# Kernel tuning notes

Hardware: AMD Instinct MI355X
Metric: run time of the kernel (lower is better)

## Reference

```python
import jax, jax.numpy as jnp
import numpy as np

N_ITEM = 100000
DIV_TRADEOFF = 0.1


def setup_inputs() -> dict:
    key = jax.random.key(0)
    ks = jax.random.split(key, 9)
    B, K, L, D_LLM, H = 512, 8, 50, 768, 128
    return {
        "user_id": jax.random.randint(ks[0], (B,), 0, 50000),
        "base_model_preds": jax.random.randint(ks[1], (B, K, L), 0, N_ITEM + 1),
        "preference_in": jax.random.normal(ks[2], (B, H), jnp.float32),
        "pos_label": jax.random.normal(ks[3], (B, K), jnp.float32),
        "neg_label": jax.random.normal(ks[4], (B, K), jnp.float32),
        "user_embeddings": jax.random.normal(ks[5], (50000, H), jnp.float32) * 0.01,
        "item_embeddings": jax.random.normal(ks[6], (N_ITEM + 1, D_LLM), jnp.float32) * 0.02,
        "W_proj": jax.random.normal(ks[7], (D_LLM, H), jnp.float32) * (1.0 / np.sqrt(D_LLM)),
        "b_proj": jax.random.normal(ks[8], (H,), jnp.float32) * 0.01,
    }


def reference(user_id, base_model_preds, preference_in, pos_label, neg_label,
              user_embeddings, item_embeddings, W_proj, b_proj):
    B, K, L = base_model_preds.shape
    # masked gather-embed: ids outside (0, n_item] map to a zero row
    valid = (base_model_preds > 0) & (base_model_preds <= N_ITEM)
    safe_ids = jnp.where(valid, base_model_preds, 0)
    focus_llm = item_embeddings[safe_ids] * valid[..., None].astype(item_embeddings.dtype)  # [B,K,L,D_llm]
    # linear projection to hidden (bias applied everywhere, matching nn.Linear on zeroed rows)
    bm = jnp.einsum('bkld,dh->bklh', focus_llm, W_proj) + b_proj  # [B,K,L,H]
    # time-decay weighted sum over sequence positions
    time_w = 1.0 / jnp.log2(jnp.arange(L, dtype=jnp.float32) + 2.0)  # [L]
    basemodel_emb = jnp.einsum('bklh,l->bkh', bm, time_w)  # [B,K,H]
    # preference = DIEN(...) + user_emb  (DIEN output modeled by preference_in)
    preference = preference_in + user_embeddings[user_id]  # [B,H]
    wgts_org = jnp.einsum('bkh,bh->bk', basemodel_emb, preference)
    wgts = jax.nn.softmax(wgts_org, axis=-1)  # [B,K]
    pos_scores = jnp.sum(pos_label * wgts, axis=1)
    neg_scores = jnp.sum(neg_label * wgts, axis=1)
    loss = -jnp.sum(jax.nn.log_sigmoid(pos_scores - neg_scores))
    # diversity regularizer (use_div=True)
    cov_wgt = jax.lax.stop_gradient(wgts[:, None, :] + wgts[:, :, None])  # [B,K,K]
    cov_mask = 1.0 - jnp.eye(K, dtype=wgts.dtype)  # [K,K]
    gram = jnp.einsum('bih,bjh->bij', basemodel_emb, basemodel_emb) ** 2
    loss_div = DIV_TRADEOFF * jnp.mean(cov_mask[None] * gram * cov_wgt)
    return loss + loss_div
```

## Files before the change

kernel.cpp:

```cpp
#include <hip/hip_runtime.h>
#include <math.h>

#define B_SZ 512
#define K_SZ 8
#define L_SZ 50
#define DLLM 768
#define H_SZ 128
#define N_ITEM 100000
#define DIV_TRADEOFF 0.1f
#define M_PAD 100032

typedef float  f32x4 __attribute__((ext_vector_type(4)));
typedef short  bf16x8 __attribute__((ext_vector_type(8)));
typedef unsigned int u32x4 __attribute__((ext_vector_type(4)));
typedef unsigned short u16x8 __attribute__((ext_vector_type(8)));

__device__ __forceinline__ unsigned short f2bf(float f) {
    unsigned u = __float_as_uint(f);
    u += 0x7fffu + ((u >> 16) & 1u);
    return (unsigned short)(u >> 16);
}

__device__ __forceinline__ void gload_lds16(const void* g, void* l) {
    __builtin_amdgcn_global_load_lds(
        (const __attribute__((address_space(1))) unsigned*)g,
        (__attribute__((address_space(3))) unsigned*)l, 16, 0, 0);
}

__global__ __launch_bounds__(256) void k_wt(
    const float* __restrict__ W,
    unsigned short* __restrict__ Wt,
    float* __restrict__ out)
{
    __shared__ float tile[64][65];
    const int kb = blockIdx.x >> 1;
    const int nb = blockIdx.x & 1;
    const int t  = threadIdx.x;
    if (blockIdx.x == 0 && t == 0) out[0] = 0.0f;

    const int r  = t >> 2;
    const int c0 = (t & 3) * 16;
    #pragma unroll
    for (int j = 0; j < 4; ++j) {
        const float4 v = *(const float4*)(W + (size_t)(kb * 64 + r) * H_SZ + nb * 64 + c0 + j * 4);
        tile[r][c0 + j * 4 + 0] = v.x;
        tile[r][c0 + j * 4 + 1] = v.y;
        tile[r][c0 + j * 4 + 2] = v.z;
        tile[r][c0 + j * 4 + 3] = v.w;
    }
    __syncthreads();
    const int n  = t >> 2;
    const int k0 = (t & 3) * 16;
    u16x8 lo, hi;
    #pragma unroll
    for (int j = 0; j < 8; ++j) lo[j] = f2bf(tile[k0 + j][n]);
    #pragma unroll
    for (int j = 0; j < 8; ++j) hi[j] = f2bf(tile[k0 + 8 + j][n]);
    unsigned short* dst = Wt + (size_t)(nb * 64 + n) * DLLM + kb * 64 + k0;
    *(u16x8*)(dst)     = lo;
    *(u16x8*)(dst + 8) = hi;
}

__global__ __launch_bounds__(256) void k_proj(
    const float* __restrict__ item,
    const unsigned short* __restrict__ Wt,
    unsigned short* __restrict__ projb)
{
    __shared__ float          As[2][64 * 64];
    __shared__ unsigned short Bs[2][128 * 64];

    const int t    = threadIdx.x;
    const int brow = blockIdx.x * 64;
    const int w    = t >> 6;
    const int lane = t & 63;
    const int nl   = lane & 15;
    const int g    = lane >> 4;
    const int key  = nl & 7;

    const int a_rsub = (lane >> 4);
    const int a_gl   = lane & 15;
    const int b_nsub = (lane >> 3);
    const int b_gl   = lane & 7;
    const int b_key  = b_nsub & 7;

    const int r = w * 16 + nl;

    auto STAGE = [&](int d, int c) {
        const int kc = c * 64;
        #pragma unroll
        for (int i = 0; i < 4; ++i) {
            const int row_t = w * 16 + i * 4 + a_rsub;
            const int rowS  = (brow + row_t <= N_ITEM) ? (brow + row_t) : N_ITEM;
            const int ka    = (a_gl ^ (row_t & 7)) * 4;
            gload_lds16(item + (size_t)rowS * DLLM + kc + ka,
                        &As[d][w * 1024 + i * 256]);
        }
        #pragma unroll
        for (int i = 0; i < 4; ++i) {
            const int n_t = w * 32 + i * 8 + b_nsub;
            const int kb  = (b_gl ^ b_key) * 8;
            gload_lds16(Wt + (size_t)n_t * DLLM + kc + kb,
                        &Bs[d][w * 2048 + i * 512]);
        }
    };

    f32x4 acc[8];
    #pragma unroll
    for (int i = 0; i < 8; ++i) acc[i] = (f32x4){0.f, 0.f, 0.f, 0.f};

    STAGE(0, 0);

    for (int c = 0; c < 12; ++c) {
        const int cur = c & 1;
        if (c < 11) STAGE(cur ^ 1, c + 1);
        if (c < 11) asm volatile("s_waitcnt vmcnt(8)" ::: "memory");
        else        asm volatile("s_waitcnt vmcnt(0)" ::: "memory");
        __builtin_amdgcn_s_barrier();
        __builtin_amdgcn_sched_barrier(0);

        #pragma unroll
        for (int ks = 0; ks < 2; ++ks) {
            const f32x4 alo = *(const f32x4*)&As[cur][r * 64 + 4 * ((ks * 8 + 2 * g)     ^ key)];
            const f32x4 ahi = *(const f32x4*)&As[cur][r * 64 + 4 * ((ks * 8 + 2 * g + 1) ^ key)];
            unsigned p0, p1, p2, p3;
            asm("v_cvt_pk_bf16_f32 %0, %1, %2" : "=v"(p0) : "v"(alo.x), "v"(alo.y));
            asm("v_cvt_pk_bf16_f32 %0, %1, %2" : "=v"(p1) : "v"(alo.z), "v"(alo.w));
            asm("v_cvt_pk_bf16_f32 %0, %1, %2" : "=v"(p2) : "v"(ahi.x), "v"(ahi.y));
            asm("v_cvt_pk_bf16_f32 %0, %1, %2" : "=v"(p3) : "v"(ahi.z), "v"(ahi.w));
            union { u32x4 u; bf16x8 s; } af;
            af.u[0] = p0; af.u[1] = p1; af.u[2] = p2; af.u[3] = p3;

            #pragma unroll
            for (int nt = 0; nt < 8; ++nt) {
                const bf16x8 b = *(const bf16x8*)&Bs[cur][(nt * 16 + nl) * 64
                                                          + 8 * ((ks * 4 + g) ^ key)];
                acc[nt] = __builtin_amdgcn_mfma_f32_16x16x32_bf16(af.s, b, acc[nt], 0, 0, 0);
            }
        }
        asm volatile("s_waitcnt lgkmcnt(0)" ::: "memory");
        __builtin_amdgcn_s_barrier();
        __builtin_amdgcn_sched_barrier(0);
    }

    const int rbase = brow + w * 16 + 4 * g;
    #pragma unroll
    for (int nt = 0; nt < 8; ++nt) {
        #pragma unroll
        for (int rr = 0; rr < 4; ++rr) {
            projb[(size_t)(rbase + rr) * H_SZ + nt * 16 + nl] = f2bf(acc[nt][rr]);
        }
    }
}

__global__ __launch_bounds__(256) void k_gather2(
    const int* __restrict__ preds,
    const unsigned short* __restrict__ projb,
    const float* __restrict__ bproj,
    float* __restrict__ emb)
{
    const int wv   = threadIdx.x >> 6;
    const int lane = threadIdx.x & 63;
    const int bk   = blockIdx.x * 4 + wv;
    const int h2   = lane * 2;
    const int* __restrict__ p = preds + (size_t)bk * L_SZ;

    constexpr int PF = 8;
    unsigned buf[PF];
    float wgt[PF];
    #pragma unroll
    for (int i = 0; i < PF; ++i) {
        const int id = p[i];
        const bool v = (id > 0) && (id <= N_ITEM);
        wgt[i] = v ? (1.0f / log2f((float)(i + 2))) : 0.0f;
        buf[i] = *(const unsigned*)(projb + (size_t)(v ? id : 0) * H_SZ + h2);
    }
    float a0 = 0.f, a1 = 0.f;
    #pragma unroll
    for (int l = 0; l < L_SZ; ++l) {
        const int s = l % PF;
        const unsigned u = buf[s];
        const float w = wgt[s];
        if (l + PF < L_SZ) {
            const int id = p[l + PF];
            const bool v = (id > 0) && (id <= N_ITEM);
            wgt[s] = v ? (1.0f / log2f((float)(l + PF + 2))) : 0.0f;
            buf[s] = *(const unsigned*)(projb + (size_t)(v ? id : 0) * H_SZ + h2);
        }
        a0 += w * __uint_as_float(u << 16);
        a1 += w * __uint_as_float(u & 0xffff0000u);
    }
    float sumw = 0.f;
    #pragma unroll
    for (int l = 0; l < L_SZ; ++l) sumw += 1.0f / log2f((float)(l + 2));
    float2 o;
    o.x = a0 + bproj[h2]     * sumw;
    o.y = a1 + bproj[h2 + 1] * sumw;
    *(float2*)(emb + (size_t)bk * H_SZ + h2) = o;
}

__global__ __launch_bounds__(256) void k_loss(
    const int* __restrict__ user_id, const float* __restrict__ pref_in,
    const float* __restrict__ pos_label, const float* __restrict__ neg_label,
    const float* __restrict__ user_emb, const float* __restrict__ emb,
    float* __restrict__ out)
{
    const int b = blockIdx.x;
    const int tid = threadIdx.x;
    __shared__ float pref[H_SZ];
    __shared__ float e[K_SZ][H_SZ + 1];
    __shared__ float sdot[K_SZ];
    __shared__ float wg[K_SZ];
    __shared__ float lossb_s;
    if (tid < H_SZ) {
        const int uid = user_id[b];
        pref[tid] = pref_in[(size_t)b * H_SZ + tid] + user_emb[(size_t)uid * H_SZ + tid];
    }
    const float* eb = emb + (size_t)b * K_SZ * H_SZ;
    #pragma unroll
    for (int i = 0; i < 4; ++i) {
        const int idx = tid * 4 + i;
        e[idx >> 7][idx & (H_SZ - 1)] = eb[idx];
    }
    __syncthreads();
    {
        const int k = tid >> 5;
        const int lane = tid & 31;
        float s = e[k][lane] * pref[lane] + e[k][lane + 32] * pref[lane + 32]
                + e[k][lane + 64] * pref[lane + 64] + e[k][lane + 96] * pref[lane + 96];
        #pragma unroll
        for (int m = 16; m >= 1; m >>= 1) s += __shfl_xor(s, m, 64);
        if (lane == 0) sdot[k] = s;
    }
    __syncthreads();
    if (tid == 0) {
        float mx = sdot[0];
        #pragma unroll
        for (int k = 1; k < K_SZ; ++k) mx = fmaxf(mx, sdot[k]);
        float sum = 0.f; float ex[K_SZ];
        #pragma unroll
        for (int k = 0; k < K_SZ; ++k) { ex[k] = expf(sdot[k] - mx); sum += ex[k]; }
        float ps = 0.f, ns = 0.f;
        #pragma unroll
        for (int k = 0; k < K_SZ; ++k) {
            const float w = ex[k] / sum;
            wg[k] = w;
            ps += pos_label[(size_t)b * K_SZ + k] * w;
            ns += neg_label[(size_t)b * K_SZ + k] * w;
        }
        const float x = ps - ns;
        lossb_s = fmaxf(-x, 0.f) + log1pf(expf(-fabsf(x)));
    }
    __syncthreads();
    if (tid < 64) {
        const int i = tid >> 3;
        const int j = tid & 7;
        float g = 0.f;
        for (int h = 0; h < H_SZ; ++h) g += e[i][h] * e[j][h];
        float v = (i != j) ? (g * g * (wg[i] + wg[j])) : 0.f;
        #pragma unroll
        for (int m = 32; m >= 1; m >>= 1) v += __shfl_xor(v, m, 64);
        if (tid == 0) {
            const float mean_div = v / (float)(B_SZ * K_SZ * K_SZ);
            atomicAdd(out, lossb_s + DIV_TRADEOFF * mean_div);
        }
    }
}

__global__ __launch_bounds__(192) void k_gather_fb(
    const int* __restrict__ preds, const float* __restrict__ item,
    float* __restrict__ wf, float* __restrict__ out)
{
    const int bk  = blockIdx.x;
    const int tid = threadIdx.x;
    if (bk == 0 && tid == 0) out[0] = 0.0f;
    const int* __restrict__ p = preds + (size_t)bk * L_SZ;
    const float* __restrict__ ibase = item + (size_t)tid * 4;
    float4 acc = make_float4(0.f, 0.f, 0.f, 0.f);
    constexpr int PF = 8;
    float4 buf[PF]; float wgt[PF];
    #pragma unroll
    for (int i = 0; i < PF; ++i) {
        const int id = p[i];
        const bool v = (id > 0) && (id <= N_ITEM);
        wgt[i] = v ? (1.0f / log2f((float)(i + 2))) : 0.0f;
        buf[i] = *(const float4*)(ibase + (size_t)(v ? id : 0) * DLLM);
    }
    #pragma unroll
    for (int l = 0; l < L_SZ; ++l) {
        const int s = l % PF;
        const float4 v4 = buf[s];
        const float  w  = wgt[s];
        if (l + PF < L_SZ) {
            const int id = p[l + PF];
            const bool v = (id > 0) && (id <= N_ITEM);
            wgt[s] = v ? (1.0f / log2f((float)(l + PF + 2))) : 0.0f;
            buf[s] = *(const float4*)(ibase + (size_t)(v ? id : 0) * DLLM);
        }
        acc.x += w * v4.x; acc.y += w * v4.y; acc.z += w * v4.z; acc.w += w * v4.w;
    }
    *(float4*)(wf + (size_t)bk * DLLM + (size_t)tid * 4) = acc;
}

__global__ __launch_bounds__(256) void k_projloss_fb(
    const float* __restrict__ wf, const float* __restrict__ W,
    const float* __restrict__ bproj, const int* __restrict__ user_id,
    const float* __restrict__ pref_in, const float* __restrict__ pos_label,
    const float* __restrict__ neg_label, const float* __restrict__ user_emb,
    float* __restrict__ out)
{
    const int b   = blockIdx.x;
    const int tid = threadIdx.x;
    const int c   = tid & (H_SZ - 1);
    const int rg  = tid >> 7;
    __shared__ float A[K_SZ][H_SZ];
    __shared__ float e[K_SZ][H_SZ + 1];
    __shared__ float pref[H_SZ];
    __shared__ float sdot[K_SZ];
    __shared__ float wg[K_SZ];
    __shared__ float lossb_s;
    float acc[4] = {0.f, 0.f, 0.f, 0.f};
    const size_t rowbase = (size_t)b * K_SZ;
    for (int kb = 0; kb < DLLM; kb += H_SZ) {
        __syncthreads();
        {
            const int r  = tid >> 5;
            const int kk = (tid & 31) * 4;
            *(float4*)&A[r][kk] = *(const float4*)(wf + (rowbase + r) * DLLM + kb + kk);
        }
        __syncthreads();
        #pragma unroll 4
        for (int k = 0; k < H_SZ; k += 4) {
            const float4 a0 = *(const float4*)&A[rg][k];
            const float4 a1 = *(const float4*)&A[rg + 2][k];
            const float4 a2 = *(const float4*)&A[rg + 4][k];
            const float4 a3 = *(const float4*)&A[rg + 6][k];
            const float* Wp = W + (size_t)(kb + k) * H_SZ + c;
            const float w0 = Wp[0]; const float w1 = Wp[H_SZ];
            const float w2 = Wp[2 * H_SZ]; const float w3 = Wp[3 * H_SZ];
            acc[0] += a0.x * w0 + a0.y * w1 + a0.z * w2 + a0.w * w3;
            acc[1] += a1.x * w0 + a1.y * w1 + a1.z * w2 + a1.w * w3;
            acc[2] += a2.x * w0 + a2.y * w1 + a2.z * w2 + a2.w * w3;
            acc[3] += a3.x * w0 + a3.y * w1 + a3.z * w2 + a3.w * w3;
        }
    }
    float sumw = 0.f;
    #pragma unroll
    for (int l = 0; l < L_SZ; ++l) sumw += 1.0f / log2f((float)(l + 2));
    const float bterm = bproj[c] * sumw;
    #pragma unroll
    for (int ri = 0; ri < 4; ++ri) e[rg + 2 * ri][c] = acc[ri] + bterm;
    if (tid < H_SZ) {
        const int uid = user_id[b];
        pref[tid] = pref_in[(size_t)b * H_SZ + tid] + user_emb[(size_t)uid * H_SZ + tid];
    }
    __syncthreads();
    {
        const int k    = tid >> 5;
        const int lane = tid & 31;
        float s = e[k][lane] * pref[lane] + e[k][lane + 32] * pref[lane + 32]
                + e[k][lane + 64] * pref[lane + 64] + e[k][lane + 96] * pref[lane + 96];
        #pragma unroll
        for (int m = 16; m >= 1; m >>= 1) s += __shfl_xor(s, m, 64);
        if (lane == 0) sdot[k] = s;
    }
    __syncthreads();
    if (tid == 0) {
        float mx = sdot[0];
        #pragma unroll
        for (int k = 1; k < K_SZ; ++k) mx = fmaxf(mx, sdot[k]);
        float sum = 0.f; float ex[K_SZ];
        #pragma unroll
        for (int k = 0; k < K_SZ; ++k) { ex[k] = expf(sdot[k] - mx); sum += ex[k]; }
        float ps = 0.f, ns = 0.f;
        #pragma unroll
        for (int k = 0; k < K_SZ; ++k) {
            const float w = ex[k] / sum;
            wg[k] = w;
            ps += pos_label[(size_t)b * K_SZ + k] * w;
            ns += neg_label[(size_t)b * K_SZ + k] * w;
        }
        const float x = ps - ns;
        lossb_s = fmaxf(-x, 0.f) + log1pf(expf(-fabsf(x)));
    }
    __syncthreads();
    if (tid < 64) {
        const int i = tid >> 3;
        const int j = tid & 7;
        float g = 0.f;
        for (int h = 0; h < H_SZ; ++h) g += e[i][h] * e[j][h];
        float v = (i != j) ? (g * g * (wg[i] + wg[j])) : 0.f;
        #pragma unroll
        for (int m = 32; m >= 1; m >>= 1) v += __shfl_xor(v, m, 64);
        if (tid == 0) {
            const float mean_div = v / (float)(B_SZ * K_SZ * K_SZ);
            atomicAdd(out, lossb_s + DIV_TRADEOFF * mean_div);
        }
    }
}

extern "C" void kernel_launch(void* const* d_in, const int* in_sizes, int n_in,
                              void* d_out, int out_size, void* d_ws, size_t ws_size,
                              hipStream_t stream) {
    const int*   user_id   = (const int*)  d_in[0];
    const int*   preds     = (const int*)  d_in[1];
    const float* pref_in   = (const float*)d_in[2];
    const float* pos_label = (const float*)d_in[3];
    const float* neg_label = (const float*)d_in[4];
    const float* user_emb  = (const float*)d_in[5];
    const float* item_emb  = (const float*)d_in[6];
    const float* W_proj    = (const float*)d_in[7];
    const float* b_proj    = (const float*)d_in[8];

    float* out = (float*)d_out;

    const size_t projb_bytes = (size_t)M_PAD * H_SZ * sizeof(unsigned short);
    const size_t wt_off      = projb_bytes;
    const size_t wt_bytes    = (size_t)H_SZ * DLLM * sizeof(unsigned short);
    const size_t emb_off     = wt_off + wt_bytes;
    const size_t emb_bytes   = (size_t)B_SZ * K_SZ * H_SZ * sizeof(float);
    const size_t need        = emb_off + emb_bytes;

    if (ws_size >= need) {
        unsigned short* projb = (unsigned short*)d_ws;
        unsigned short* Wt    = (unsigned short*)((char*)d_ws + wt_off);
        float*          emb   = (float*)((char*)d_ws + emb_off);

        k_wt<<<24, 256, 0, stream>>>(W_proj, Wt, out);
        k_proj<<<M_PAD / 64, 256, 0, stream>>>(item_emb, Wt, projb);
        k_gather2<<<B_SZ * K_SZ / 4, 256, 0, stream>>>(preds, projb, b_proj, emb);
        k_loss<<<B_SZ, 256, 0, stream>>>(user_id, pref_in, pos_label, neg_label,
                                         user_emb, emb, out);
    } else {
        float* wf = (float*)d_ws;
        k_gather_fb<<<B_SZ * K_SZ, 192, 0, stream>>>(preds, item_emb, wf, out);
        k_projloss_fb<<<B_SZ, 256, 0, stream>>>(wf, W_proj, b_proj, user_id, pref_in,
                                                pos_label, neg_label, user_emb, out);
    }
}
```

Before: 107.8 us.

## Preload bf16 A tile once per block in k_proj and fuse gather with loss

k_proj now loads the full 32-row slice of item embeddings up front, converts it to bf16 once and keeps all of K in LDS. This removes the per-k-step fp32 A staging and repeated conversions, and the block now uses 32 rows with four waves splitting the N dimension. The gather and loss kernels are fused into one 512-thread block per batch row, which drops the intermediate emb buffer and one launch. The trade-offs are a larger LDS footprint per block, less overlap of A loads with compute, and a higher occupancy target of two blocks per CU.

```diff
diff --git a/kernel.cpp b/kernel.cpp
--- a/kernel.cpp
+++ b/kernel.cpp
@@ -61,40 +61,28 @@
     *(u16x8*)(dst + 8) = hi;
 }
 
-__global__ __launch_bounds__(256) void k_proj(
+__global__ __launch_bounds__(256, 2) void k_proj(
     const float* __restrict__ item,
     const unsigned short* __restrict__ Wt,
     unsigned short* __restrict__ projb)
 {
-    __shared__ float          As[2][64 * 64];
+    __shared__ unsigned short As[32 * DLLM];
     __shared__ unsigned short Bs[2][128 * 64];
 
     const int t    = threadIdx.x;
-    const int brow = blockIdx.x * 64;
+    const int brow = blockIdx.x * 32;
     const int w    = t >> 6;
     const int lane = t & 63;
     const int nl   = lane & 15;
     const int g    = lane >> 4;
     const int key  = nl & 7;
 
-    const int a_rsub = (lane >> 4);
-    const int a_gl   = lane & 15;
     const int b_nsub = (lane >> 3);
     const int b_gl   = lane & 7;
     const int b_key  = b_nsub & 7;
 
-    const int r = w * 16 + nl;
-
-    auto STAGE = [&](int d, int c) {
+    auto STAGE_B = [&](int d, int c) {
         const int kc = c * 64;
-        #pragma unroll
-        for (int i = 0; i < 4; ++i) {
-            const int row_t = w * 16 + i * 4 + a_rsub;
-            const int rowS  = (brow + row_t <= N_ITEM) ? (brow + row_t) : N_ITEM;
-            const int ka    = (a_gl ^ (row_t & 7)) * 4;
-            gload_lds16(item + (size_t)rowS * DLLM + kc + ka,
-                        &As[d][w * 1024 + i * 256]);
-        }
         #pragma unroll
         for (int i = 0; i < 4; ++i) {
             const int n_t = w * 32 + i * 8 + b_nsub;
@@ -104,37 +92,55 @@
         }
     };
 
-    f32x4 acc[8];
-    #pragma unroll
-    for (int i = 0; i < 8; ++i) acc[i] = (f32x4){0.f, 0.f, 0.f, 0.f};
-
-    STAGE(0, 0);
+    STAGE_B(0, 0);
+
+    {
+        f32x4 L[24];
+        #pragma unroll
+        for (int j = 0; j < 24; ++j) {
+            const int row_g = brow + w * 8 + j / 3;
+            const int rowS  = (row_g <= N_ITEM) ? row_g : N_ITEM;
+            L[j] = *(const f32x4*)(item + (size_t)rowS * DLLM + (j % 3) * 256 + lane * 4);
+        }
+        #pragma unroll
+        for (int j = 0; j < 24; ++j) {
+            unsigned p0, p1;
+            asm("v_cvt_pk_bf16_f32 %0, %1, %2" : "=v"(p0) : "v"(L[j].x), "v"(L[j].y));
+            asm("v_cvt_pk_bf16_f32 %0, %1, %2" : "=v"(p1) : "v"(L[j].z), "v"(L[j].w));
+            const int row_l = w * 8 + j / 3;
+            const int rk    = (j / 3) & 7;
+            const int pos   = (j % 3) * 32 + ((lane >> 1) ^ rk);
+            uint2 d; d.x = p0; d.y = p1;
+            *(uint2*)((char*)As + row_l * (DLLM * 2) + pos * 16 + (lane & 1) * 8) = d;
+        }
+    }
+    __syncthreads();
+
+    const int arow = (w & 1) * 16 + nl;
+    const int nth  = (w >> 1) * 4;
+
+    f32x4 acc[4];
+    #pragma unroll
+    for (int i = 0; i < 4; ++i) acc[i] = (f32x4){0.f, 0.f, 0.f, 0.f};
 
     for (int c = 0; c < 12; ++c) {
         const int cur = c & 1;
-        if (c < 11) STAGE(cur ^ 1, c + 1);
-        if (c < 11) asm volatile("s_waitcnt vmcnt(8)" ::: "memory");
+        if (c < 11) STAGE_B(cur ^ 1, c + 1);
+        if (c < 11) asm volatile("s_waitcnt vmcnt(4)" ::: "memory");
         else        asm volatile("s_waitcnt vmcnt(0)" ::: "memory");
         __builtin_amdgcn_s_barrier();
         __builtin_amdgcn_sched_barrier(0);
 
         #pragma unroll
         for (int ks = 0; ks < 2; ++ks) {
-            const f32x4 alo = *(const f32x4*)&As[cur][r * 64 + 4 * ((ks * 8 + 2 * g)     ^ key)];
-            const f32x4 ahi = *(const f32x4*)&As[cur][r * 64 + 4 * ((ks * 8 + 2 * g + 1) ^ key)];
-            unsigned p0, p1, p2, p3;
-            asm("v_cvt_pk_bf16_f32 %0, %1, %2" : "=v"(p0) : "v"(alo.x), "v"(alo.y));
-            asm("v_cvt_pk_bf16_f32 %0, %1, %2" : "=v"(p1) : "v"(alo.z), "v"(alo.w));
-            asm("v_cvt_pk_bf16_f32 %0, %1, %2" : "=v"(p2) : "v"(ahi.x), "v"(ahi.y));
-            asm("v_cvt_pk_bf16_f32 %0, %1, %2" : "=v"(p3) : "v"(ahi.z), "v"(ahi.w));
-            union { u32x4 u; bf16x8 s; } af;
-            af.u[0] = p0; af.u[1] = p1; af.u[2] = p2; af.u[3] = p3;
-
+            const int q = (ks * 4 + g) ^ key;
+            const bf16x8 af = *(const bf16x8*)((char*)As
+                                + arow * (DLLM * 2) + (c * 8 + q) * 16);
             #pragma unroll
-            for (int nt = 0; nt < 8; ++nt) {
-                const bf16x8 b = *(const bf16x8*)&Bs[cur][(nt * 16 + nl) * 64
-                                                          + 8 * ((ks * 4 + g) ^ key)];
-                acc[nt] = __builtin_amdgcn_mfma_f32_16x16x32_bf16(af.s, b, acc[nt], 0, 0, 0);
+            for (int nt = 0; nt < 4; ++nt) {
+                const bf16x8 b = *(const bf16x8*)&Bs[cur][((nth + nt) * 16 + nl) * 64
+                                                          + 8 * q];
+                acc[nt] = __builtin_amdgcn_mfma_f32_16x16x32_bf16(af, b, acc[nt], 0, 0, 0);
             }
         }
         asm volatile("s_waitcnt lgkmcnt(0)" ::: "memory");
@@ -142,96 +148,87 @@
         __builtin_amdgcn_sched_barrier(0);
     }
 
-    const int rbase = brow + w * 16 + 4 * g;
-    #pragma unroll
-    for (int nt = 0; nt < 8; ++nt) {
+    const int rbase = brow + (w & 1) * 16 + 4 * g;
+    #pragma unroll
+    for (int nt = 0; nt < 4; ++nt) {
         #pragma unroll
         for (int rr = 0; rr < 4; ++rr) {
-            projb[(size_t)(rbase + rr) * H_SZ + nt * 16 + nl] = f2bf(acc[nt][rr]);
-        }
-    }
-}
-
-__global__ __launch_bounds__(256) void k_gather2(
+            projb[(size_t)(rbase + rr) * H_SZ + (nth + nt) * 16 + nl] = f2bf(acc[nt][rr]);
+        }
+    }
+}
+
+__global__ __launch_bounds__(512) void k_gloss(
     const int* __restrict__ preds,
     const unsigned short* __restrict__ projb,
     const float* __restrict__ bproj,
-    float* __restrict__ emb)
-{
-    const int wv   = threadIdx.x >> 6;
-    const int lane = threadIdx.x & 63;
-    const int bk   = blockIdx.x * 4 + wv;
-    const int h2   = lane * 2;
-    const int* __restrict__ p = preds + (size_t)bk * L_SZ;
-
-    constexpr int PF = 8;
-    unsigned buf[PF];
-    float wgt[PF];
-    #pragma unroll
-    for (int i = 0; i < PF; ++i) {
-        const int id = p[i];
-        const bool v = (id > 0) && (id <= N_ITEM);
-        wgt[i] = v ? (1.0f / log2f((float)(i + 2))) : 0.0f;
-        buf[i] = *(const unsigned*)(projb + (size_t)(v ? id : 0) * H_SZ + h2);
-    }
-    float a0 = 0.f, a1 = 0.f;
-    #pragma unroll
-    for (int l = 0; l < L_SZ; ++l) {
-        const int s = l % PF;
-        const unsigned u = buf[s];
-        const float w = wgt[s];
-        if (l + PF < L_SZ) {
-            const int id = p[l + PF];
-            const bool v = (id > 0) && (id <= N_ITEM);
-            wgt[s] = v ? (1.0f / log2f((float)(l + PF + 2))) : 0.0f;
-            buf[s] = *(const unsigned*)(projb + (size_t)(v ? id : 0) * H_SZ + h2);
-        }
-        a0 += w * __uint_as_float(u << 16);
-        a1 += w * __uint_as_float(u & 0xffff0000u);
-    }
-    float sumw = 0.f;
-    #pragma unroll
-    for (int l = 0; l < L_SZ; ++l) sumw += 1.0f / log2f((float)(l + 2));
-    float2 o;
-    o.x = a0 + bproj[h2]     * sumw;
-    o.y = a1 + bproj[h2 + 1] * sumw;
-    *(float2*)(emb + (size_t)bk * H_SZ + h2) = o;
-}
-
-__global__ __launch_bounds__(256) void k_loss(
     const int* __restrict__ user_id, const float* __restrict__ pref_in,
     const float* __restrict__ pos_label, const float* __restrict__ neg_label,
-    const float* __restrict__ user_emb, const float* __restrict__ emb,
+    const float* __restrict__ user_emb,
     float* __restrict__ out)
 {
-    const int b = blockIdx.x;
-    const int tid = threadIdx.x;
+    const int b    = blockIdx.x;
+    const int tid  = threadIdx.x;
+    const int wv   = tid >> 6;
+    const int lane = tid & 63;
+    const int h2   = lane * 2;
+
+    __shared__ float e[K_SZ][H_SZ + 1];
     __shared__ float pref[H_SZ];
-    __shared__ float e[K_SZ][H_SZ + 1];
     __shared__ float sdot[K_SZ];
     __shared__ float wg[K_SZ];
     __shared__ float lossb_s;
+
+    {
+        const int* __restrict__ p = preds + ((size_t)b * K_SZ + wv) * L_SZ;
+        constexpr int PF = 8;
+        unsigned buf[PF];
+        float wgt[PF];
+        #pragma unroll
+        for (int i = 0; i < PF; ++i) {
+            const int id = p[i];
+            const bool v = (id > 0) && (id <= N_ITEM);
+            wgt[i] = v ? (1.0f / log2f((float)(i + 2))) : 0.0f;
+            buf[i] = *(const unsigned*)(projb + (size_t)(v ? id : 0) * H_SZ + h2);
+        }
+        float a0 = 0.f, a1 = 0.f;
+        #pragma unroll
+        for (int l = 0; l < L_SZ; ++l) {
+            const int s = l % PF;
+            const unsigned u = buf[s];
+            const float w = wgt[s];
+            if (l + PF < L_SZ) {
+                const int id = p[l + PF];
+                const bool v = (id > 0) && (id <= N_ITEM);
+                wgt[s] = v ? (1.0f / log2f((float)(l + PF + 2))) : 0.0f;
+                buf[s] = *(const unsigned*)(projb + (size_t)(v ? id : 0) * H_SZ + h2);
+            }
+            a0 += w * __uint_as_float(u << 16);
+            a1 += w * __uint_as_float(u & 0xffff0000u);
+        }
+        float sumw = 0.f;
+        #pragma unroll
+        for (int l = 0; l < L_SZ; ++l) sumw += 1.0f / log2f((float)(l + 2));
+        e[wv][h2]     = a0 + bproj[h2]     * sumw;
+        e[wv][h2 + 1] = a1 + bproj[h2 + 1] * sumw;
+    }
     if (tid < H_SZ) {
         const int uid = user_id[b];
         pref[tid] = pref_in[(size_t)b * H_SZ + tid] + user_emb[(size_t)uid * H_SZ + tid];
     }
-    const float* eb = emb + (size_t)b * K_SZ * H_SZ;
-    #pragma unroll
-    for (int i = 0; i < 4; ++i) {
-        const int idx = tid * 4 + i;
-        e[idx >> 7][idx & (H_SZ - 1)] = eb[idx];
-    }
-    __syncthreads();
-    {
+    __syncthreads();
+
+    if (tid < 256) {
         const int k = tid >> 5;
-        const int lane = tid & 31;
-        float s = e[k][lane] * pref[lane] + e[k][lane + 32] * pref[lane + 32]
-                + e[k][lane + 64] * pref[lane + 64] + e[k][lane + 96] * pref[lane + 96];
+        const int l32 = tid & 31;
+        float s = e[k][l32] * pref[l32] + e[k][l32 + 32] * pref[l32 + 32]
+                + e[k][l32 + 64] * pref[l32 + 64] + e[k][l32 + 96] * pref[l32 + 96];
         #pragma unroll
         for (int m = 16; m >= 1; m >>= 1) s += __shfl_xor(s, m, 64);
-        if (lane == 0) sdot[k] = s;
-    }
-    __syncthreads();
+        if (l32 == 0) sdot[k] = s;
+    }
+    __syncthreads();
+
     if (tid == 0) {
         float mx = sdot[0];
         #pragma unroll
@@ -251,12 +248,13 @@
         lossb_s = fmaxf(-x, 0.f) + log1pf(expf(-fabsf(x)));
     }
     __syncthreads();
+
     if (tid < 64) {
         const int i = tid >> 3;
         const int j = tid & 7;
-        float g = 0.f;
-        for (int h = 0; h < H_SZ; ++h) g += e[i][h] * e[j][h];
-        float v = (i != j) ? (g * g * (wg[i] + wg[j])) : 0.f;
+        float gsum = 0.f;
+        for (int h = 0; h < H_SZ; ++h) gsum += e[i][h] * e[j][h];
+        float v = (i != j) ? (gsum * gsum * (wg[i] + wg[j])) : 0.f;
         #pragma unroll
         for (int m = 32; m >= 1; m >>= 1) v += __shfl_xor(v, m, 64);
         if (tid == 0) {
@@ -416,20 +414,16 @@
     const size_t projb_bytes = (size_t)M_PAD * H_SZ * sizeof(unsigned short);
     const size_t wt_off      = projb_bytes;
     const size_t wt_bytes    = (size_t)H_SZ * DLLM * sizeof(unsigned short);
-    const size_t emb_off     = wt_off + wt_bytes;
-    const size_t emb_bytes   = (size_t)B_SZ * K_SZ * H_SZ * sizeof(float);
-    const size_t need        = emb_off + emb_bytes;
+    const size_t need        = wt_off + wt_bytes;
 
     if (ws_size >= need) {
         unsigned short* projb = (unsigned short*)d_ws;
         unsigned short* Wt    = (unsigned short*)((char*)d_ws + wt_off);
-        float*          emb   = (float*)((char*)d_ws + emb_off);
 
         k_wt<<<24, 256, 0, stream>>>(W_proj, Wt, out);
-        k_proj<<<M_PAD / 64, 256, 0, stream>>>(item_emb, Wt, projb);
-        k_gather2<<<B_SZ * K_SZ / 4, 256, 0, stream>>>(preds, projb, b_proj, emb);
-        k_loss<<<B_SZ, 256, 0, stream>>>(user_id, pref_in, pos_label, neg_label,
-                                         user_emb, emb, out);
+        k_proj<<<M_PAD / 32, 256, 0, stream>>>(item_emb, Wt, projb);
+        k_gloss<<<B_SZ, 512, 0, stream>>>(preds, projb, b_proj, user_id, pref_in,
+                                          pos_label, neg_label, user_emb, out);
     } else {
         float* wf = (float*)d_ws;
         k_gather_fb<<<B_SZ * K_SZ, 192, 0, stream>>>(preds, item_emb, wf, out);
```

Result: slower. 120.9 us (+12.2%).
